# Optimization experiments

Hardware: AMD Instinct MI355X
Metric: run time of the kernel (lower is better)

## Reference

```python
import jax, jax.numpy as jnp
import numpy as np

# Problem dimensions (match init_kwargs / input_specs)
B, NT = 4, 256          # shots, timesteps
NZ, NX = 384, 384       # domain
NREC = 128              # receivers
DT, DH = 0.001, 10.0    # time step [s], grid spacing [m]


def setup_inputs() -> dict:
    key = jax.random.key(0)
    k1, k2, k3, k4, k5, k6 = jax.random.split(key, 6)
    # source wavelets, one per shot: [B, NT]
    x = jax.random.normal(k1, (B, NT), dtype=jnp.float32)
    # velocity model 1500..3500 m/s: [NZ, NX]
    vp = 1500.0 + 2000.0 * jax.random.uniform(k2, (NZ, NX), dtype=jnp.float32)
    # per-shot source locations (kept away from the boundary)
    src_y = jax.random.randint(k3, (B,), 20, NZ - 20, dtype=jnp.int32)
    src_x = jax.random.randint(k4, (B,), 20, NX - 20, dtype=jnp.int32)
    # shared receiver array
    rec_y = jax.random.randint(k5, (NREC,), 20, NZ - 20, dtype=jnp.int32)
    rec_x = jax.random.randint(k6, (NREC,), 20, NX - 20, dtype=jnp.int32)
    return {"x": x, "vp": vp, "src_y": src_y, "src_x": src_x,
            "rec_y": rec_y, "rec_x": rec_x}


def _laplacian(u, inv_dh2):
    # 5-point stencil with zero (Dirichlet) boundaries; u: [B, NZ, NX]
    l = (u[:, 2:, 1:-1] + u[:, :-2, 1:-1]
         + u[:, 1:-1, 2:] + u[:, 1:-1, :-2]
         - 4.0 * u[:, 1:-1, 1:-1]) * inv_dh2
    return jnp.pad(l, ((0, 0), (1, 1), (1, 1)))


def reference(x, vp, src_y, src_x, rec_y, rec_x):
    """Second-order acoustic wave time-stepping with scatter source injection
    and receiver gather, as in WaveRNN.forward. Returns [NT, B, NREC] traces."""
    c2dt2 = (vp * DT) ** 2            # [NZ, NX], broadcast over shots
    inv_dh2 = jnp.float32(1.0 / (DH * DH))
    bidx = jnp.arange(B)

    def step(carry, xt):
        h1, h2 = carry                # current / previous wavefields [B,NZ,NX]
        hn = 2.0 * h1 - h2 + c2dt2 * _laplacian(h1, inv_dh2)
        hn = hn.at[bidx, src_y, src_x].add(xt)   # source injection (smask scatter)
        rec = hn[:, rec_y, rec_x]                 # receiver gather [B, NREC]
        return (hn, h1), rec

    h0 = jnp.zeros((B, NZ, NX), dtype=x.dtype)
    (_, _), y = jax.lax.scan(jax.checkpoint(step), (h0, h0), x.T)  # scan over time
    return y  # [NT, B, NREC]
```

## Files before the change

kernel.cpp:

```cpp
#include <hip/hip_runtime.h>

#define BB 4
#define NT 256
#define NZ 384
#define NX 384
#define NREC 128
#define NZX (NZ*NX)
#define BNZX (BB*NZX)
#define DT 0.001f
#define INV_DH2 0.01f

#define TILE 48
#define HALO 8
#define REGN 64
#define NBLK 256
#define NTHR 512
#define FSTRIDE 16

__global__ void wave_init(unsigned* flags) {
    int i = blockIdx.x * blockDim.x + threadIdx.x;
    if (i < NBLK * FSTRIDE) flags[i] = 0u;
}

__device__ inline float dpp_shl1(float v) {
    return __int_as_float(__builtin_amdgcn_update_dpp(
        0, __float_as_int(v), 0x130 , 0xf, 0xf, true));
}
__device__ inline float dpp_shr1(float v) {
    return __int_as_float(__builtin_amdgcn_update_dpp(
        0, __float_as_int(v), 0x138 , 0xf, 0xf, true));
}

__device__ inline void stg2(unsigned long long* p, float a, float b) {
    unsigned long long v = (unsigned long long)__float_as_uint(a)
                         | ((unsigned long long)__float_as_uint(b) << 32);
    __hip_atomic_store(p, v, __ATOMIC_RELAXED, __HIP_MEMORY_SCOPE_AGENT);
}
__device__ inline unsigned long long ldg2(const unsigned long long* p) {
    return __hip_atomic_load(p, __ATOMIC_RELAXED, __HIP_MEMORY_SCOPE_AGENT);
}

__global__ __launch_bounds__(NTHR)
void wave_tiled(float* __restrict__ ws, const float* __restrict__ vp,
                const float* __restrict__ x,
                const int* __restrict__ src_y, const int* __restrict__ src_x,
                const int* __restrict__ rec_y, const int* __restrict__ rec_x,
                float* __restrict__ y) {
    __shared__ float bnd[2][16][REGN];
    __shared__ float recBuf[NREC][8];
    __shared__ float xs[NT];
    __shared__ int recLoc[NREC], recOut[NREC];
    __shared__ int recCnt;

    unsigned* flags = (unsigned*)(ws + 4*BNZX);
    unsigned long long* F[2] = { (unsigned long long*)ws,
                                 (unsigned long long*)ws + BNZX };

    const int tid = threadIdx.x;
    const int col = tid & 63;
    const int w   = tid >> 6;
    const int r0  = w << 3;
    const int blk = blockIdx.x;
    const int b  = blk >> 6;
    const int tz = (blk >> 3) & 7;
    const int tx = blk & 7;
    const int oz = tz*TILE - HALO, ox = tx*TILE - HALO;
    const int gx = ox + col;
    const int sy = src_y[b], sx = src_x[b];

    if (tid == 0) recCnt = 0;
    for (int k = tid; k < 16*REGN; k += NTHR) ((float*)bnd[0])[k] = 0.f;
    for (int k = tid; k < NT; k += NTHR) xs[k] = x[b*NT + k];
    __syncthreads();
    for (int r = tid; r < NREC; r += NTHR) {
        int ry = rec_y[r], rx = rec_x[r];
        if (ry/TILE == tz && rx/TILE == tx) {
            int p = atomicAdd(&recCnt, 1);
            recLoc[p] = ((ry - oz) << 6) | (rx - ox);
            recOut[p] = b*NREC + r;
        }
    }
    __syncthreads();

    int myN = 0, myM[4], myP[4];
    bool ovf = false;
    for (int p = 0; p < recCnt; ++p) {
        int rl = recLoc[p];
        if ((rl & 63) == col) {
            int rm = (rl >> 6) - r0;
            if ((unsigned)rm < 8u) {
                if (myN < 4) { myM[myN] = rm; myP[myN] = p; ++myN; }
                else ovf = true;
            }
        }
    }

    int nbId = blk;
    if (tid < 8) {
        int d = tid + (tid >= 4);
        int nz2 = tz + d/3 - 1, nx2 = tx + d%3 - 1;
        if ((unsigned)nz2 < 8u && (unsigned)nx2 < 8u)
            nbId = (b << 6) | (nz2 << 3) | nx2;
    }

    float cur[8], prv[8], c2i[8];
    #pragma unroll
    for (int m = 0; m < 8; ++m) {
        cur[m] = 0.f; prv[m] = 0.f;
        const int gz = oz + r0 + m;
        const bool inner = (gz > 0 && gz < NZ-1 && gx > 0 && gx < NX-1);
        const float v = inner ? vp[gz*NX + gx] * DT : 0.f;
        c2i[m] = v * v * INV_DH2;
    }
    const bool srcCol = (gx == sx);
    const int  srcM   = sy - oz - r0;
    const int  iuUp   = (2*w-1 < 0) ? 0 : 2*w-1;
    const int  iuDn   = (2*w+2 > 15) ? 15 : 2*w+2;
    const bool gxIn = (gx >= 0 && gx < NX);
    const int  gxc  = min(max(gx, 0), NX-1);
    __syncthreads();

    #pragma unroll 1
    for (int t = 0; t < NT; ++t) {
        const int pr = t & 1, pw = pr ^ 1;
        const float upB = bnd[pr][iuUp][col];
        const float dnB = bnd[pr][iuDn][col];

        float hn[8];
        #pragma unroll
        for (int m = 0; m < 8; ++m) {
            const float ce = cur[m];
            const float up = (m == 0) ? upB : cur[m-1];
            const float dn = (m == 7) ? dnB : cur[m+1];
            const float lf = dpp_shl1(ce);
            const float rt = dpp_shr1(ce);
            const float s  = (up + dn) + (lf + rt);
            hn[m] = fmaf(2.f, ce, -prv[m]) + c2i[m] * fmaf(-4.f, ce, s);
        }
        #pragma unroll
        for (int m = 0; m < 8; ++m) { prv[m] = cur[m]; cur[m] = hn[m]; }

        if (srcCol && (unsigned)srcM < 8u) {
            const float xv = xs[t];
            #pragma unroll
            for (int m = 0; m < 8; ++m) if (m == srcM) cur[m] += xv;
        }
        {
            const int s2 = t & 7;
            if (ovf) {
                for (int p = 0; p < recCnt; ++p) {
                    int rl = recLoc[p];
                    if ((rl & 63) == col) {
                        int rm = (rl >> 6) - r0;
                        if ((unsigned)rm < 8u) {
                            float v = cur[0];
                            #pragma unroll
                            for (int m = 1; m < 8; ++m) if (rm == m) v = cur[m];
                            recBuf[p][s2] = v;
                        }
                    }
                }
            } else {
                #pragma unroll
                for (int k = 0; k < 4; ++k) {
                    if (k < myN) {
                        float v = cur[0];
                        #pragma unroll
                        for (int m = 1; m < 8; ++m) if (myM[k] == m) v = cur[m];
                        recBuf[myP[k]][s2] = v;
                    }
                }
            }
        }
        bnd[pw][2*w  ][col] = cur[0];
        bnd[pw][2*w+1][col] = cur[7];

        if ((t & 7) == 7) {
            const int o = t >> 3;
            if (t < NT-1) {
                unsigned long long* Fw = F[o & 1];
                const bool colF = (col >= HALO   && col < REGN-HALO);
                const bool colM = (col >= 2*HALO && col < REGN-2*HALO);
                #pragma unroll
                for (int m = 0; m < 8; ++m) {
                    const int i = r0 + m;
                    const bool rowF = (i >= HALO   && i < REGN-HALO);
                    const bool rowM = (i >= 2*HALO && i < REGN-2*HALO);
                    if (colF && rowF && !(colM && rowM))
                        stg2(&Fw[(size_t)b*NZX + (size_t)(oz+i)*NX + gx],
                             cur[m], prv[m]);
                }
                __syncthreads();
                if (tid < 64) {
                    if (tid == 0)
                        __hip_atomic_store(&flags[blk * FSTRIDE], (unsigned)(o+1),
                                           __ATOMIC_RELAXED, __HIP_MEMORY_SCOPE_AGENT);
                    for (;;) {
                        unsigned f = __hip_atomic_load(&flags[nbId * FSTRIDE],
                                         __ATOMIC_RELAXED, __HIP_MEMORY_SCOPE_AGENT);
                        if (__all(f >= (unsigned)(o+1))) break;
                    }
                } else {
                    for (int k = tid - 64; k < recCnt*8; k += NTHR - 64) {
                        int p = k >> 3, s2 = k & 7;
                        y[(size_t)((o<<3)+s2)*(BB*NREC) + recOut[p]] = recBuf[p][s2];
                    }
                }
                __syncthreads();
                const bool colH = (col < HALO || col >= REGN-HALO);
                unsigned long long tmp[8];
                bool ringm[8], valm[8];
                #pragma unroll
                for (int m = 0; m < 8; ++m) {
                    const int i = r0 + m;
                    const int gz = oz + i;
                    ringm[m] = colH || i < HALO || i >= REGN-HALO;
                    valm[m]  = gxIn && gz >= 0 && gz < NZ;
                    const int gzc = min(max(gz, 0), NZ-1);
                    if (ringm[m])
                        tmp[m] = ldg2(&Fw[(size_t)b*NZX + (size_t)gzc*NX + gxc]);
                }
                #pragma unroll
                for (int m = 0; m < 8; ++m) {
                    if (ringm[m]) {
                        cur[m] = valm[m] ? __uint_as_float((unsigned)tmp[m]) : 0.f;
                        prv[m] = valm[m] ? __uint_as_float((unsigned)(tmp[m] >> 32)) : 0.f;
                    }
                }
                bnd[pw][2*w  ][col] = cur[0];
                bnd[pw][2*w+1][col] = cur[7];
            } else {
                __syncthreads();
                for (int k = tid; k < recCnt*8; k += NTHR) {
                    int p = k >> 3, s2 = k & 7;
                    y[(size_t)((o<<3)+s2)*(BB*NREC) + recOut[p]] = recBuf[p][s2];
                }
            }
        }
        __syncthreads();
    }
}

extern "C" void kernel_launch(void* const* d_in, const int* in_sizes, int n_in,
                              void* d_out, int out_size, void* d_ws, size_t ws_size,
                              hipStream_t stream) {
    const float* x     = (const float*)d_in[0];
    const float* vp    = (const float*)d_in[1];
    const int*   src_y = (const int*)d_in[2];
    const int*   src_x = (const int*)d_in[3];
    const int*   rec_y = (const int*)d_in[4];
    const int*   rec_x = (const int*)d_in[5];
    float* y  = (float*)d_out;
    float* ws = (float*)d_ws;

    wave_init<<<(NBLK*FSTRIDE + 255)/256, 256, 0, stream>>>((unsigned*)(ws + 4*BNZX));
    wave_tiled<<<NBLK, NTHR, 0, stream>>>(ws, vp, x, src_y, src_x, rec_y, rec_x, y);
}
```

Measured before the change: 275.5 us.

## Replace block barriers with per-wave shared and global flag synchronization

Removes every-step __syncthreads and the block-level neighbor flag handshake. Each wave now signals its own progress through an LDS flag and spins only on its vertical neighbor waves. At exchange steps it publishes a per-wave global flag and waits only on the specific neighbor waves in adjacent tiles whose halo it needs. The aim is to let waves drift independently and cut barrier stalls, but it adds spin-loop traffic, and the relaxed-ordering correctness around the double-buffered boundary and global halo buffers is delicate.

```diff
diff --git a/kernel.cpp b/kernel.cpp
--- a/kernel.cpp
+++ b/kernel.cpp
@@ -16,10 +16,11 @@
 #define NBLK 256
 #define NTHR 512
 #define FSTRIDE 16
-
-__global__ void wave_init(unsigned* flags) {
+#define NGFLAG (NBLK*8*FSTRIDE)
+
+__global__ void wave_init(unsigned* gflags) {
     int i = blockIdx.x * blockDim.x + threadIdx.x;
-    if (i < NBLK * FSTRIDE) flags[i] = 0u;
+    if (i < NGFLAG) gflags[i] = 0u;
 }
 
 __device__ inline float dpp_shl1(float v) {
@@ -37,6 +38,9 @@
     __hip_atomic_store(p, v, __ATOMIC_RELAXED, __HIP_MEMORY_SCOPE_AGENT);
 }
 __device__ inline unsigned long long ldg2(const unsigned long long* p) {
+    return __hip_atomic_load(p, __ATOMIC_RELAXED, __HIP_MEMORY_SCOPE_AGENT);
+}
+__device__ inline unsigned ldflag(const unsigned* p) {
     return __hip_atomic_load(p, __ATOMIC_RELAXED, __HIP_MEMORY_SCOPE_AGENT);
 }
 
@@ -51,8 +55,9 @@
     __shared__ float xs[NT];
     __shared__ int recLoc[NREC], recOut[NREC];
     __shared__ int recCnt;
-
-    unsigned* flags = (unsigned*)(ws + 4*BNZX);
+    __shared__ int wflag[8];
+
+    unsigned* gflags = (unsigned*)(ws + 4*BNZX);
     unsigned long long* F[2] = { (unsigned long long*)ws,
                                  (unsigned long long*)ws + BNZX };
 
@@ -69,7 +74,8 @@
     const int sy = src_y[b], sx = src_x[b];
 
     if (tid == 0) recCnt = 0;
-    for (int k = tid; k < 16*REGN; k += NTHR) ((float*)bnd[0])[k] = 0.f;
+    if (tid < 8) wflag[tid] = 0;
+    for (int k = tid; k < 2*16*REGN; k += NTHR) ((float*)bnd)[k] = 0.f;
     for (int k = tid; k < NT; k += NTHR) xs[k] = x[b*NT + k];
     __syncthreads();
     for (int r = tid; r < NREC; r += NTHR) {
@@ -95,12 +101,23 @@
         }
     }
 
-    int nbId = blk;
-    if (tid < 8) {
-        int d = tid + (tid >= 4);
-        int nz2 = tz + d/3 - 1, nx2 = tx + d%3 - 1;
-        if ((unsigned)nz2 < 8u && (unsigned)nx2 < 8u)
-            nbId = (b << 6) | (nz2 << 3) | nx2;
+    const int self = blk*8 + w;
+    int g0 = self, g1 = self, g2 = self;
+    if (w == 0) {
+        if (tz > 0) {
+            g0 = (((b<<6)|((tz-1)<<3)|tx))*8 + 6;
+            if (tx > 0) g1 = (((b<<6)|((tz-1)<<3)|(tx-1)))*8 + 6;
+            if (tx < 7) g2 = (((b<<6)|((tz-1)<<3)|(tx+1)))*8 + 6;
+        }
+    } else if (w == 7) {
+        if (tz < 7) {
+            g0 = (((b<<6)|((tz+1)<<3)|tx))*8 + 1;
+            if (tx > 0) g1 = (((b<<6)|((tz+1)<<3)|(tx-1)))*8 + 1;
+            if (tx < 7) g2 = (((b<<6)|((tz+1)<<3)|(tx+1)))*8 + 1;
+        }
+    } else {
+        if (tx > 0) g0 = (((b<<6)|(tz<<3)|(tx-1)))*8 + w;
+        if (tx < 7) g1 = (((b<<6)|(tz<<3)|(tx+1)))*8 + w;
     }
 
     float cur[8], prv[8], c2i[8];
@@ -116,12 +133,21 @@
     const int  srcM   = sy - oz - r0;
     const int  iuUp   = (2*w-1 < 0) ? 0 : 2*w-1;
     const int  iuDn   = (2*w+2 > 15) ? 15 : 2*w+2;
-    const bool gxIn = (gx >= 0 && gx < NX);
-    const int  gxc  = min(max(gx, 0), NX-1);
+    const bool gxIn   = (gx >= 0 && gx < NX);
+    const int  gxc    = min(max(gx, 0), NX-1);
+    const bool spinUp = (w > 0), spinDn = (w < 7);
+    volatile int* vf = wflag;
     __syncthreads();
 
     #pragma unroll 1
     for (int t = 0; t < NT; ++t) {
+        for (;;) {
+            bool ok = true;
+            if (spinUp) ok = ok && (vf[w-1] >= t);
+            if (spinDn) ok = ok && (vf[w+1] >= t);
+            if (ok) break;
+        }
+        __threadfence_block();
         const int pr = t & 1, pw = pr ^ 1;
         const float upB = bnd[pr][iuUp][col];
         const float dnB = bnd[pr][iuDn][col];
@@ -172,12 +198,17 @@
                 }
             }
         }
-        bnd[pw][2*w  ][col] = cur[0];
-        bnd[pw][2*w+1][col] = cur[7];
 
         if ((t & 7) == 7) {
             const int o = t >> 3;
+            for (int k = col; k < recCnt*8; k += 64) {
+                int p = k >> 3, s2 = k & 7;
+                int rr = recLoc[p] >> 6;
+                if (rr >= r0 && rr < r0 + 8)
+                    y[(size_t)((o<<3)+s2)*(BB*NREC) + recOut[p]] = recBuf[p][s2];
+            }
             if (t < NT-1) {
+                __syncthreads();
                 unsigned long long* Fw = F[o & 1];
                 const bool colF = (col >= HALO   && col < REGN-HALO);
                 const bool colM = (col >= 2*HALO && col < REGN-2*HALO);
@@ -190,23 +221,18 @@
                         stg2(&Fw[(size_t)b*NZX + (size_t)(oz+i)*NX + gx],
                              cur[m], prv[m]);
                 }
-                __syncthreads();
-                if (tid < 64) {
-                    if (tid == 0)
-                        __hip_atomic_store(&flags[blk * FSTRIDE], (unsigned)(o+1),
-                                           __ATOMIC_RELAXED, __HIP_MEMORY_SCOPE_AGENT);
-                    for (;;) {
-                        unsigned f = __hip_atomic_load(&flags[nbId * FSTRIDE],
-                                         __ATOMIC_RELAXED, __HIP_MEMORY_SCOPE_AGENT);
-                        if (__all(f >= (unsigned)(o+1))) break;
-                    }
-                } else {
-                    for (int k = tid - 64; k < recCnt*8; k += NTHR - 64) {
-                        int p = k >> 3, s2 = k & 7;
-                        y[(size_t)((o<<3)+s2)*(BB*NREC) + recOut[p]] = recBuf[p][s2];
-                    }
-                }
-                __syncthreads();
+                __builtin_amdgcn_s_waitcnt(0x0f70);
+                if (col == 0)
+                    __hip_atomic_store(&gflags[self * FSTRIDE], (unsigned)(o+1),
+                                       __ATOMIC_RELAXED, __HIP_MEMORY_SCOPE_AGENT);
+                const unsigned tgt = (unsigned)(o + 1);
+                for (;;) {
+                    unsigned f0 = ldflag(&gflags[g0 * FSTRIDE]);
+                    unsigned f1 = ldflag(&gflags[g1 * FSTRIDE]);
+                    unsigned f2 = ldflag(&gflags[g2 * FSTRIDE]);
+                    if (f0 >= tgt && f1 >= tgt && f2 >= tgt) break;
+                    __builtin_amdgcn_s_sleep(1);
+                }
                 const bool colH = (col < HALO || col >= REGN-HALO);
                 unsigned long long tmp[8];
                 bool ringm[8], valm[8];
@@ -227,17 +253,12 @@
                         prv[m] = valm[m] ? __uint_as_float((unsigned)(tmp[m] >> 32)) : 0.f;
                     }
                 }
-                bnd[pw][2*w  ][col] = cur[0];
-                bnd[pw][2*w+1][col] = cur[7];
-            } else {
-                __syncthreads();
-                for (int k = tid; k < recCnt*8; k += NTHR) {
-                    int p = k >> 3, s2 = k & 7;
-                    y[(size_t)((o<<3)+s2)*(BB*NREC) + recOut[p]] = recBuf[p][s2];
-                }
-            }
-        }
-        __syncthreads();
+            }
+        }
+        bnd[pw][2*w  ][col] = cur[0];
+        bnd[pw][2*w+1][col] = cur[7];
+        __threadfence_block();
+        if (col == 0) wflag[w] = t + 1;
     }
 }
 
@@ -253,6 +274,6 @@
     float* y  = (float*)d_out;
     float* ws = (float*)d_ws;
 
-    wave_init<<<(NBLK*FSTRIDE + 255)/256, 256, 0, stream>>>((unsigned*)(ws + 4*BNZX));
+    wave_init<<<(NGFLAG + 255)/256, 256, 0, stream>>>((unsigned*)(ws + 4*BNZX));
     wave_tiled<<<NBLK, NTHR, 0, stream>>>(ws, vp, x, src_y, src_x, rec_y, rec_x, y);
 }
```

Result: slower. 354.4 us (+28.7%).

## Split domain into 512 smaller z-tiles with 5 waves and planar halo buffers

Applied to the files above, without the earlier changes.

Changes the temporal-blocking decomposition from 256 blocks of 48x48 tiles (64x64 regions, 8 waves) to 512 blocks of 24x48 tiles (40x64 regions, 5 waves), doubling the number of persistent blocks to spread work over more CUs. The halo exchange buffer layout moves from interleaved 64-bit cur/prv pairs to two separate float planes with 32-bit atomic loads and stores. The smaller tiles raise the redundant halo compute fraction, and the higher block count means more flag synchronization and requires all 512 blocks to be co-resident.

```diff
diff --git a/kernel.cpp b/kernel.cpp
--- a/kernel.cpp
+++ b/kernel.cpp
@@ -10,11 +10,16 @@
 #define DT 0.001f
 #define INV_DH2 0.01f
 
-#define TILE 48
+#define TZN 24
+#define TXN 48
 #define HALO 8
-#define REGN 64
-#define NBLK 256
-#define NTHR 512
+#define RZN 40
+#define RXN 64
+#define NTBZ 16
+#define NTBX 8
+#define NBLK 512
+#define NWAVE 5
+#define NTHR (NWAVE*64)
 #define FSTRIDE 16
 
 __global__ void wave_init(unsigned* flags) {
@@ -30,13 +35,13 @@
     return __int_as_float(__builtin_amdgcn_update_dpp(
         0, __float_as_int(v), 0x138 , 0xf, 0xf, true));
 }
-
-__device__ inline void stg2(unsigned long long* p, float a, float b) {
-    unsigned long long v = (unsigned long long)__float_as_uint(a)
-                         | ((unsigned long long)__float_as_uint(b) << 32);
+__device__ inline float ldgf(const float* p) {
+    return __hip_atomic_load(p, __ATOMIC_RELAXED, __HIP_MEMORY_SCOPE_AGENT);
+}
+__device__ inline void stgf(float* p, float v) {
     __hip_atomic_store(p, v, __ATOMIC_RELAXED, __HIP_MEMORY_SCOPE_AGENT);
 }
-__device__ inline unsigned long long ldg2(const unsigned long long* p) {
+__device__ inline unsigned ldflag(const unsigned* p) {
     return __hip_atomic_load(p, __ATOMIC_RELAXED, __HIP_MEMORY_SCOPE_AGENT);
 }
 
@@ -46,35 +51,35 @@
                 const int* __restrict__ src_y, const int* __restrict__ src_x,
                 const int* __restrict__ rec_y, const int* __restrict__ rec_x,
                 float* __restrict__ y) {
-    __shared__ float bnd[2][16][REGN];
+    __shared__ float bnd[2][2*NWAVE][RXN];
     __shared__ float recBuf[NREC][8];
     __shared__ float xs[NT];
     __shared__ int recLoc[NREC], recOut[NREC];
     __shared__ int recCnt;
 
     unsigned* flags = (unsigned*)(ws + 4*BNZX);
-    unsigned long long* F[2] = { (unsigned long long*)ws,
-                                 (unsigned long long*)ws + BNZX };
+    float* F0 = ws;
+    float* F1 = ws + 2*BNZX;
 
     const int tid = threadIdx.x;
     const int col = tid & 63;
     const int w   = tid >> 6;
     const int r0  = w << 3;
     const int blk = blockIdx.x;
-    const int b  = blk >> 6;
-    const int tz = (blk >> 3) & 7;
+    const int b  = blk >> 7;
+    const int tz = (blk >> 3) & 15;
     const int tx = blk & 7;
-    const int oz = tz*TILE - HALO, ox = tx*TILE - HALO;
+    const int oz = tz*TZN - HALO, ox = tx*TXN - HALO;
     const int gx = ox + col;
     const int sy = src_y[b], sx = src_x[b];
 
     if (tid == 0) recCnt = 0;
-    for (int k = tid; k < 16*REGN; k += NTHR) ((float*)bnd[0])[k] = 0.f;
+    for (int k = tid; k < 2*2*NWAVE*RXN; k += NTHR) ((float*)bnd)[k] = 0.f;
     for (int k = tid; k < NT; k += NTHR) xs[k] = x[b*NT + k];
     __syncthreads();
     for (int r = tid; r < NREC; r += NTHR) {
         int ry = rec_y[r], rx = rec_x[r];
-        if (ry/TILE == tz && rx/TILE == tx) {
+        if (ry/TZN == tz && rx/TXN == tx) {
             int p = atomicAdd(&recCnt, 1);
             recLoc[p] = ((ry - oz) << 6) | (rx - ox);
             recOut[p] = b*NREC + r;
@@ -99,8 +104,8 @@
     if (tid < 8) {
         int d = tid + (tid >= 4);
         int nz2 = tz + d/3 - 1, nx2 = tx + d%3 - 1;
-        if ((unsigned)nz2 < 8u && (unsigned)nx2 < 8u)
-            nbId = (b << 6) | (nz2 << 3) | nx2;
+        if ((unsigned)nz2 < (unsigned)NTBZ && (unsigned)nx2 < (unsigned)NTBX)
+            nbId = (b << 7) | (nz2 << 3) | nx2;
     }
 
     float cur[8], prv[8], c2i[8];
@@ -115,9 +120,9 @@
     const bool srcCol = (gx == sx);
     const int  srcM   = sy - oz - r0;
     const int  iuUp   = (2*w-1 < 0) ? 0 : 2*w-1;
-    const int  iuDn   = (2*w+2 > 15) ? 15 : 2*w+2;
-    const bool gxIn = (gx >= 0 && gx < NX);
-    const int  gxc  = min(max(gx, 0), NX-1);
+    const int  iuDn   = (2*w+2 > 2*NWAVE-1) ? 2*NWAVE-1 : 2*w+2;
+    const bool gxIn   = (gx >= 0 && gx < NX);
+    const int  gxc    = min(max(gx, 0), NX-1);
     __syncthreads();
 
     #pragma unroll 1
@@ -178,17 +183,20 @@
         if ((t & 7) == 7) {
             const int o = t >> 3;
             if (t < NT-1) {
-                unsigned long long* Fw = F[o & 1];
-                const bool colF = (col >= HALO   && col < REGN-HALO);
-                const bool colM = (col >= 2*HALO && col < REGN-2*HALO);
+                float* Gc = (o & 1) ? F1 : F0;
+                float* Gp = Gc + BNZX;
+                const bool colF = (col >= HALO   && col < RXN-HALO);
+                const bool colM = (col >= 2*HALO && col < RXN-2*HALO);
                 #pragma unroll
                 for (int m = 0; m < 8; ++m) {
                     const int i = r0 + m;
-                    const bool rowF = (i >= HALO   && i < REGN-HALO);
-                    const bool rowM = (i >= 2*HALO && i < REGN-2*HALO);
-                    if (colF && rowF && !(colM && rowM))
-                        stg2(&Fw[(size_t)b*NZX + (size_t)(oz+i)*NX + gx],
-                             cur[m], prv[m]);
+                    const bool rowF = (i >= HALO   && i < RZN-HALO);
+                    const bool rowM = (i >= 2*HALO && i < RZN-2*HALO);
+                    if (colF && rowF && !(colM && rowM)) {
+                        const size_t g = (size_t)b*NZX + (size_t)(oz+i)*NX + gx;
+                        stgf(&Gc[g], cur[m]);
+                        stgf(&Gp[g], prv[m]);
+                    }
                 }
                 __syncthreads();
                 if (tid < 64) {
@@ -196,8 +204,7 @@
                         __hip_atomic_store(&flags[blk * FSTRIDE], (unsigned)(o+1),
                                            __ATOMIC_RELAXED, __HIP_MEMORY_SCOPE_AGENT);
                     for (;;) {
-                        unsigned f = __hip_atomic_load(&flags[nbId * FSTRIDE],
-                                         __ATOMIC_RELAXED, __HIP_MEMORY_SCOPE_AGENT);
+                        unsigned f = ldflag(&flags[nbId * FSTRIDE]);
                         if (__all(f >= (unsigned)(o+1))) break;
                     }
                 } else {
@@ -207,24 +214,27 @@
                     }
                 }
                 __syncthreads();
-                const bool colH = (col < HALO || col >= REGN-HALO);
-                unsigned long long tmp[8];
+                const bool colH = (col < HALO || col >= RXN-HALO);
+                float tc[8], tp[8];
                 bool ringm[8], valm[8];
                 #pragma unroll
                 for (int m = 0; m < 8; ++m) {
                     const int i = r0 + m;
                     const int gz = oz + i;
-                    ringm[m] = colH || i < HALO || i >= REGN-HALO;
+                    ringm[m] = colH || i < HALO || i >= RZN-HALO;
                     valm[m]  = gxIn && gz >= 0 && gz < NZ;
                     const int gzc = min(max(gz, 0), NZ-1);
-                    if (ringm[m])
-                        tmp[m] = ldg2(&Fw[(size_t)b*NZX + (size_t)gzc*NX + gxc]);
+                    if (ringm[m]) {
+                        const size_t g = (size_t)b*NZX + (size_t)gzc*NX + gxc;
+                        tc[m] = ldgf(&Gc[g]);
+                        tp[m] = ldgf(&Gp[g]);
+                    }
                 }
                 #pragma unroll
                 for (int m = 0; m < 8; ++m) {
                     if (ringm[m]) {
-                        cur[m] = valm[m] ? __uint_as_float((unsigned)tmp[m]) : 0.f;
-                        prv[m] = valm[m] ? __uint_as_float((unsigned)(tmp[m] >> 32)) : 0.f;
+                        cur[m] = valm[m] ? tc[m] : 0.f;
+                        prv[m] = valm[m] ? tp[m] : 0.f;
                     }
                 }
                 bnd[pw][2*w  ][col] = cur[0];
```

After: 410.7 us. 49.1% more time.
